# Kernel optimization log

Measured on AMD Instinct MI355X. Metric: run time of the kernel, lower is better.

The kernel has to match this reference:

```python
import jax, jax.numpy as jnp
import numpy as np

B, T, C = 4, 2048, 768   # batch, seq, n_embd
E, K = 8, 2              # n_routed_experts, moe_top_k (expert hidden dim == C per source)


def setup_inputs() -> dict:
    key = jax.random.key(0)
    ks = jax.random.split(key, 6)
    s = 0.02  # init scale to keep relu(x)^2 well-behaved
    return {
        "x": jax.random.normal(ks[0], (B, T, C), jnp.float32),
        "w_fc_sh": jax.random.normal(ks[1], (C, C), jnp.float32) * s,    # shared expert c_fc (stored [in,out])
        "w_proj_sh": jax.random.normal(ks[2], (C, C), jnp.float32) * s,  # shared expert c_proj
        "w1": jax.random.normal(ks[3], (E, C, C), jnp.float32) * s,      # routed experts c_fc, [E,in,out]
        "w2": jax.random.normal(ks[4], (E, C, C), jnp.float32) * s,      # routed experts c_proj
        "router_w": jax.random.normal(ks[5], (E, C), jnp.float32) * s,   # router weight [E, C]
        "balance_bias": jnp.zeros((E,), jnp.float32),                    # router balance_bias buffer
    }


def _mlp(x, wfc, wproj):
    # MLP: c_proj(relu(c_fc(x))**2)
    h = jnp.square(jax.nn.relu(x @ wfc))
    return h @ wproj


def reference(x, w_fc_sh, w_proj_sh, w1, w2, router_w, balance_bias):
    Bx, Tx, Cx = x.shape
    shared = _mlp(x, w_fc_sh, w_proj_sh)                    # [B,T,C]

    xf = x.reshape(-1, Cx)                                  # [N,C]
    # --- router ---
    logits = xf.astype(jnp.float32) @ router_w.T            # [N,E]
    scores = jax.nn.sigmoid(logits)
    _, idx = jax.lax.top_k(scores + balance_bias, K)        # selection uses biased scores
    tw = jnp.take_along_axis(scores, idx, axis=-1)          # gate weights from unbiased scores
    tw = tw / (tw.sum(-1, keepdims=True) + 1e-20)           # [N,K]

    # per-token per-expert combine weights (equivalent to gather/MLP/index_add loop)
    combine = (jax.nn.one_hot(idx, E, dtype=tw.dtype) * tw[..., None]).sum(1)  # [N,E]

    # dense all-expert compute, masked combine (same math as sparse dispatch)
    h = jnp.square(jax.nn.relu(jnp.einsum('nc,ech->neh', xf, w1)))  # [N,E,H]
    y = jnp.einsum('neh,ehc->nec', h, w2)                            # [N,E,C]
    routed = jnp.einsum('nec,ne->nc', y, combine)                    # [N,C]

    return shared + routed.reshape(Bx, Tx, Cx)
```

## Files before the change

### kernel.cpp

```cpp
#include <hip/hip_runtime.h>
#include <stdint.h>

#define N_TOK 8192
#define C_DIM 768
#define E_NUM 8
#define NT (C_DIM / 32)
#define TOTX 200
#define GRID1 1200
#define XXPX 25

typedef short short8 __attribute__((ext_vector_type(8)));
typedef __bf16 bf16x8 __attribute__((ext_vector_type(8)));
typedef float f32x4 __attribute__((ext_vector_type(4)));

static __device__ __forceinline__ unsigned short f2bf(float f) {
    unsigned u = __float_as_uint(f);
    unsigned r = u + 0x7FFFu + ((u >> 16) & 1u);
    return (unsigned short)(r >> 16);
}
static __device__ __forceinline__ float bf2f(unsigned short h) {
    return __uint_as_float(((unsigned)h) << 16);
}

__global__ void wtrans_kernel(const float* __restrict__ wfc, const float* __restrict__ wpj,
                              const float* __restrict__ w1, const float* __restrict__ w2,
                              unsigned short* __restrict__ Wt) {
    __shared__ float tile[32][33];
    const int m = blockIdx.z;
    const float* src = (m == 0) ? wfc : (m == 1) ? wpj
                     : (m < 10) ? (w1 + (size_t)(m - 2) * C_DIM * C_DIM)
                                : (w2 + (size_t)(m - 10) * C_DIM * C_DIM);
    const int i0 = blockIdx.y * 32;
    const int o0 = blockIdx.x * 32;
    #pragma unroll
    for (int rr = 0; rr < 32; rr += 8)
        tile[threadIdx.y + rr][threadIdx.x] = src[(size_t)(i0 + threadIdx.y + rr) * C_DIM + o0 + threadIdx.x];
    __syncthreads();
    unsigned short* dst = Wt + (size_t)m * C_DIM * C_DIM;
    #pragma unroll
    for (int rr = 0; rr < 32; rr += 8) {
        int o = o0 + threadIdx.y + rr;
        dst[(size_t)o * C_DIM + i0 + threadIdx.x] = f2bf(tile[threadIdx.x][threadIdx.y + rr]);
    }
}

__global__ void router_kernel(const float* __restrict__ x, const float* __restrict__ rw,
                              const float* __restrict__ bias,
                              float* __restrict__ topk_w, int* __restrict__ eids,
                              unsigned short* __restrict__ xb) {
    const int wave = threadIdx.x >> 6;
    const int lane = threadIdx.x & 63;
    const int n = blockIdx.x * 4 + wave;
    const float* xp = x + (size_t)n * C_DIM + lane * 12;
    float xv[12];
    #pragma unroll
    for (int j = 0; j < 12; j++) xv[j] = xp[j];
    unsigned short* xbp = xb + (size_t)n * C_DIM + lane * 12;
    #pragma unroll
    for (int j = 0; j < 12; j++) xbp[j] = f2bf(xv[j]);
    float acc[E_NUM];
    #pragma unroll
    for (int e = 0; e < E_NUM; e++) acc[e] = 0.f;
    #pragma unroll
    for (int e = 0; e < E_NUM; e++) {
        const float* wp = rw + (size_t)e * C_DIM + lane * 12;
        #pragma unroll
        for (int j = 0; j < 12; j++) acc[e] += xv[j] * wp[j];
    }
    #pragma unroll
    for (int e = 0; e < E_NUM; e++) {
        #pragma unroll
        for (int off = 32; off > 0; off >>= 1) acc[e] += __shfl_xor(acc[e], off, 64);
    }
    if (lane == 0) {
        float sc[E_NUM];
        #pragma unroll
        for (int e = 0; e < E_NUM; e++) sc[e] = 1.f / (1.f + expf(-acc[e]));
        int e0 = 0; float best = -1e30f;
        #pragma unroll
        for (int e = 0; e < E_NUM; e++) { float v = sc[e] + bias[e]; if (v > best) { best = v; e0 = e; } }
        int e1 = -1; float best1 = -1e30f;
        #pragma unroll
        for (int e = 0; e < E_NUM; e++) { if (e == e0) continue; float v = sc[e] + bias[e]; if (v > best1) { best1 = v; e1 = e; } }
        float w0 = sc[e0], w1 = sc[e1];
        float s = w0 + w1 + 1e-20f;
        w0 /= s; w1 /= s;
        topk_w[n * 2] = w0; topk_w[n * 2 + 1] = w1;
        eids[n * 2] = e0; eids[n * 2 + 1] = e1;
    }
}

__global__ __launch_bounds__(1024) void bucketize_kernel(const int* __restrict__ eids,
                                                         int* __restrict__ counts,
                                                         int* __restrict__ buckets) {
    const int e = blockIdx.x;
    const int t = threadIdx.x;
    const int wv = t >> 6, lane = t & 63;
    __shared__ int wave_tot[16];
    int running = 0;
    for (int start = 0; start < 2 * N_TOK; start += 1024) {
        const int i = start + t;
        const int f = (eids[i] == e) ? 1 : 0;
        unsigned long long mask = __ballot(f);
        int pre = __popcll(mask & ((1ull << lane) - 1ull));
        if (lane == 0) wave_tot[wv] = __popcll(mask);
        __syncthreads();
        int wbase = 0, tot = 0;
        #pragma unroll
        for (int j = 0; j < 16; j++) { int c = wave_tot[j]; tot += c; if (j < wv) wbase += c; }
        if (f) buckets[e * N_TOK + running + wbase + pre] = i;
        running += tot;
        __syncthreads();
    }
    if (t == 0) counts[e] = running;
}

__global__ void prefix_kernel(const int* __restrict__ counts, int* __restrict__ xoffs) {
    if (threadIdx.x == 0 && blockIdx.x == 0) {
        int a = 0;
        for (int z = 0; z < E_NUM; z++) { xoffs[z] = a; a += (counts[z] + 127) >> 7; }
        xoffs[E_NUM] = a;
        xoffs[E_NUM + 1] = a + 64;
    }
}

#define GLOAD_LDS(g, l) __builtin_amdgcn_global_load_lds((const __attribute__((address_space(1))) void*)(g), (__attribute__((address_space(3))) void*)(l), 16, 0, 0)
#define WAITVM(n) asm volatile("s_waitcnt vmcnt(" #n ")" ::: "memory")
#define SCHEDB() __builtin_amdgcn_sched_barrier(0)
#define BAR() __builtin_amdgcn_s_barrier()

template <int PHASE>
__global__ __launch_bounds__(256) void gemm_all_kernel(const unsigned short* __restrict__ Adir,
                                                       const unsigned short* __restrict__ Agat,
                                                       const unsigned short* __restrict__ WtAll,
                                                       void* __restrict__ dstDir,
                                                       unsigned short* __restrict__ dstGat,
                                                       const int* __restrict__ counts,
                                                       const int* __restrict__ buckets,
                                                       const int* __restrict__ xoffs) {
    const int fid = blockIdx.x;
    const int xcd = fid & 7;
    const int i6 = fid >> 3;
    const int xx = xcd * XXPX + i6 / 6;
    const int y = i6 % 6;
    int xo[10];
    #pragma unroll
    for (int i = 0; i < 10; i++) xo[i] = xoffs[i];
    if (xx >= xo[9]) return;
    int z = E_NUM, xl = xx - xo[8];
    #pragma unroll
    for (int zz = 0; zz < E_NUM; zz++)
        if (xx >= xo[zz] && xx < xo[zz + 1]) { z = zz; xl = xx - xo[zz]; }
    const bool sh = (z == E_NUM);
    const int rows = sh ? N_TOK : counts[z];
    const int r0 = xl * 128;
    const int c0 = y * 128;

    __shared__ __align__(16) unsigned short lds[4 * 8192];

    const int t = threadIdx.x;
    const int lane = t & 63;
    const int wv = t >> 6;
    const int wr = (wv >> 1) * 64;
    const int wc = (wv & 1) * 64;

    const int widx = sh ? (PHASE == 0 ? 0 : 1) : (PHASE == 0 ? 2 + z : 10 + z);
    const unsigned short* Bmat = WtAll + (size_t)widx * C_DIM * C_DIM;
    const int* bk = buckets + z * N_TOK;

    const int ar0 = t >> 2;
    const int ar1 = 64 + (t >> 2);
    const int acol = (((t & 3) ^ ((t >> 3) & 3)) * 8);
    int grow0, grow1;
    const unsigned short* Asrc;
    if (sh) {
        Asrc = Adir;
        grow0 = r0 + ar0; grow1 = r0 + ar1;
    } else {
        Asrc = Agat;
        int p0 = r0 + ar0, p1 = r0 + ar1;
        int e0v = bk[p0 < rows ? p0 : 0];
        int e1v = bk[p1 < rows ? p1 : 0];
        grow0 = (PHASE == 0) ? (e0v >> 1) : e0v;
        grow1 = (PHASE == 0) ? (e1v >> 1) : e1v;
    }
    const unsigned short* aptr0 = Asrc + (size_t)grow0 * C_DIM + acol;
    const unsigned short* aptr1 = Asrc + (size_t)grow1 * C_DIM + acol;
    const unsigned short* bptr0 = Bmat + (size_t)(c0 + ar0) * C_DIM + acol;
    const unsigned short* bptr1 = Bmat + (size_t)(c0 + ar1) * C_DIM + acol;

    f32x4 acc[4][4];
    #pragma unroll
    for (int i = 0; i < 4; i++)
        #pragma unroll
        for (int j = 0; j < 4; j++) acc[i][j] = (f32x4){0.f, 0.f, 0.f, 0.f};

    const int qr = (((lane >> 4) ^ ((lane >> 1) & 3)) * 8);

    {
        unsigned short* d0 = lds + t * 8;
        GLOAD_LDS(aptr0, d0);
        GLOAD_LDS(aptr1, d0 + 2048);
        GLOAD_LDS(bptr0, d0 + 4096);
        GLOAD_LDS(bptr1, d0 + 6144);
        unsigned short* d1 = lds + 8192 + t * 8;
        GLOAD_LDS(aptr0 + 32, d1);
        GLOAD_LDS(aptr1 + 32, d1 + 2048);
        GLOAD_LDS(bptr0 + 32, d1 + 4096);
        GLOAD_LDS(bptr1 + 32, d1 + 6144);
    }

    #pragma unroll
    for (int kt = 0; kt < NT; ++kt) {
        if (kt + 2 < NT) {
            unsigned short* d = lds + ((kt + 2) & 3) * 8192 + t * 8;
            const int ko = (kt + 2) * 32;
            GLOAD_LDS(aptr0 + ko, d);
            GLOAD_LDS(aptr1 + ko, d + 2048);
            GLOAD_LDS(bptr0 + ko, d + 4096);
            GLOAD_LDS(bptr1 + ko, d + 6144);
            WAITVM(8);
        } else if (kt + 2 == NT) {
            WAITVM(4);
        } else {
            WAITVM(0);
        }
        BAR();
        SCHEDB();
        const unsigned short* buf = lds + (kt & 3) * 8192;
        short8 af[4], bfr[4];
        #pragma unroll
        for (int i = 0; i < 4; i++)
            af[i] = *reinterpret_cast<const short8*>(buf + (size_t)(wr + i * 16 + (lane & 15)) * 32 + qr);
        #pragma unroll
        for (int j = 0; j < 4; j++)
            bfr[j] = *reinterpret_cast<const short8*>(buf + 4096 + (size_t)(wc + j * 16 + (lane & 15)) * 32 + qr);
        __builtin_amdgcn_s_setprio(1);
        #pragma unroll
        for (int i = 0; i < 4; i++)
            #pragma unroll
            for (int j = 0; j < 4; j++)
                acc[i][j] = __builtin_amdgcn_mfma_f32_16x16x32_bf16(
                    __builtin_bit_cast(bf16x8, af[i]), __builtin_bit_cast(bf16x8, bfr[j]), acc[i][j], 0, 0, 0);
        __builtin_amdgcn_s_setprio(0);
    }

    const int fr = lane & 15;
    const int fq = lane >> 4;
    if (sh) {
        if constexpr (PHASE == 0) {
            unsigned short* Hd = (unsigned short*)dstDir;
            #pragma unroll
            for (int i = 0; i < 4; i++)
                #pragma unroll
                for (int rr = 0; rr < 4; rr++) {
                    int n = r0 + wr + i * 16 + fq * 4 + rr;
                    size_t base = (size_t)n * C_DIM;
                    #pragma unroll
                    for (int j = 0; j < 4; j++) {
                        int col = c0 + wc + j * 16 + fr;
                        float v = acc[i][j][rr];
                        float rl = v > 0.f ? v : 0.f;
                        Hd[base + col] = f2bf(rl * rl);
                    }
                }
        } else {
            float* od = (float*)dstDir;
            #pragma unroll
            for (int i = 0; i < 4; i++)
                #pragma unroll
                for (int rr = 0; rr < 4; rr++) {
                    int n = r0 + wr + i * 16 + fq * 4 + rr;
                    size_t base = (size_t)n * C_DIM;
                    #pragma unroll
                    for (int j = 0; j < 4; j++) {
                        int col = c0 + wc + j * 16 + fr;
                        od[base + col] = acc[i][j][rr];
                    }
                }
        }
    } else {
        #pragma unroll
        for (int i = 0; i < 4; i++)
            #pragma unroll
            for (int rr = 0; rr < 4; rr++) {
                int pos = r0 + wr + i * 16 + fq * 4 + rr;
                if (pos < rows) {
                    int ent = bk[pos];
                    size_t base = (size_t)ent * C_DIM;
                    #pragma unroll
                    for (int j = 0; j < 4; j++) {
                        int col = c0 + wc + j * 16 + fr;
                        float v = acc[i][j][rr];
                        if (PHASE == 0) {
                            float rl = v > 0.f ? v : 0.f;
                            dstGat[base + col] = f2bf(rl * rl);
                        } else {
                            dstGat[base + col] = f2bf(v);
                        }
                    }
                }
            }
    }
}

__global__ void combine_kernel(float* __restrict__ out, const unsigned short* __restrict__ Y,
                               const float* __restrict__ tw) {
    int idx = blockIdx.x * blockDim.x + threadIdx.x;
    const int per_row = C_DIM / 4;
    if (idx >= N_TOK * per_row) return;
    int n = idx / per_row;
    int c = (idx % per_row) * 4;
    float w0 = tw[n * 2], w1 = tw[n * 2 + 1];
    const ushort4 a = *reinterpret_cast<const ushort4*>(Y + (size_t)(n * 2) * C_DIM + c);
    const ushort4 b = *reinterpret_cast<const ushort4*>(Y + (size_t)(n * 2 + 1) * C_DIM + c);
    float4* op = reinterpret_cast<float4*>(out + (size_t)n * C_DIM + c);
    float4 o = *op;
    o.x += w0 * bf2f(a.x) + w1 * bf2f(b.x);
    o.y += w0 * bf2f(a.y) + w1 * bf2f(b.y);
    o.z += w0 * bf2f(a.z) + w1 * bf2f(b.z);
    o.w += w0 * bf2f(a.w) + w1 * bf2f(b.w);
    *op = o;
}

extern "C" void kernel_launch(void* const* d_in, const int* in_sizes, int n_in,
                              void* d_out, int out_size, void* d_ws, size_t ws_size,
                              hipStream_t stream) {
    const float* x   = (const float*)d_in[0];
    const float* wfc = (const float*)d_in[1];
    const float* wpj = (const float*)d_in[2];
    const float* w1  = (const float*)d_in[3];
    const float* w2  = (const float*)d_in[4];
    const float* rw  = (const float*)d_in[5];
    const float* bias= (const float*)d_in[6];
    float* out = (float*)d_out;

    char* ws = (char*)d_ws;
    size_t off = 0;
    auto alloc = [&](size_t bytes) { void* p = ws + off; off += (bytes + 255) & ~(size_t)255; return p; };
    unsigned short* xb   = (unsigned short*)alloc((size_t)N_TOK * C_DIM * 2);
    unsigned short* Wt   = (unsigned short*)alloc((size_t)18 * C_DIM * C_DIM * 2);
    unsigned short* H    = (unsigned short*)alloc((size_t)N_TOK * 2 * C_DIM * 2);
    unsigned short* Hsh  = (unsigned short*)alloc((size_t)N_TOK * C_DIM * 2);
    unsigned short* Y    = (unsigned short*)alloc((size_t)N_TOK * 2 * C_DIM * 2);
    float* topk_w        = (float*)alloc((size_t)N_TOK * 2 * 4);
    int* counts          = (int*)alloc(256);
    int* buckets         = (int*)alloc((size_t)E_NUM * N_TOK * 4);
    int* eids            = (int*)alloc((size_t)2 * N_TOK * 4);
    int* xoffs           = (int*)alloc(64);

    wtrans_kernel<<<dim3(24, 24, 18), dim3(32, 8), 0, stream>>>(wfc, wpj, w1, w2, Wt);
    router_kernel<<<N_TOK / 4, 256, 0, stream>>>(x, rw, bias, topk_w, eids, xb);
    bucketize_kernel<<<E_NUM, 1024, 0, stream>>>(eids, counts, buckets);
    prefix_kernel<<<1, 64, 0, stream>>>(counts, xoffs);

    gemm_all_kernel<0><<<GRID1, 256, 0, stream>>>(xb, xb, Wt, Hsh, H, counts, buckets, xoffs);
    gemm_all_kernel<1><<<GRID1, 256, 0, stream>>>(Hsh, H, Wt, out, Y, counts, buckets, xoffs);

    combine_kernel<<<(N_TOK * (C_DIM / 4) + 255) / 256, 256, 0, stream>>>(out, Y, topk_w);
}
```

Measured before the change: 145.5 us.

## Use BK=64 double-buffered LDS pipeline in expert GEMM with 2-block occupancy hint

Changes the GEMM K-loop from 32-wide k-tiles with a 4-stage LDS ring (prefetch distance 2) to 64-wide k-tiles with two LDS buffers. Each buffer is loaded with an 8-way XOR swizzle, and the prefetch is issued right after the barrier. This halves the number of barriers and waitcnt points per tile and doubles the MFMA work between synchronisations. It also adds a launch_bounds minimum of 2 blocks per CU. The trade-off is shallower prefetch, since a full wait happens every iteration, which can expose more memory latency.

```diff
diff --git a/kernel.cpp b/kernel.cpp
--- a/kernel.cpp
+++ b/kernel.cpp
@@ -4,7 +4,7 @@
 #define N_TOK 8192
 #define C_DIM 768
 #define E_NUM 8
-#define NT (C_DIM / 32)
+#define NT2 (C_DIM / 64)
 #define TOTX 200
 #define GRID1 1200
 #define XXPX 25
@@ -125,19 +125,19 @@
 }
 
 #define GLOAD_LDS(g, l) __builtin_amdgcn_global_load_lds((const __attribute__((address_space(1))) void*)(g), (__attribute__((address_space(3))) void*)(l), 16, 0, 0)
-#define WAITVM(n) asm volatile("s_waitcnt vmcnt(" #n ")" ::: "memory")
+#define WAITVM0() asm volatile("s_waitcnt vmcnt(0)" ::: "memory")
 #define SCHEDB() __builtin_amdgcn_sched_barrier(0)
 #define BAR() __builtin_amdgcn_s_barrier()
 
 template <int PHASE>
-__global__ __launch_bounds__(256) void gemm_all_kernel(const unsigned short* __restrict__ Adir,
-                                                       const unsigned short* __restrict__ Agat,
-                                                       const unsigned short* __restrict__ WtAll,
-                                                       void* __restrict__ dstDir,
-                                                       unsigned short* __restrict__ dstGat,
-                                                       const int* __restrict__ counts,
-                                                       const int* __restrict__ buckets,
-                                                       const int* __restrict__ xoffs) {
+__global__ __launch_bounds__(256, 2) void gemm_all_kernel(const unsigned short* __restrict__ Adir,
+                                                          const unsigned short* __restrict__ Agat,
+                                                          const unsigned short* __restrict__ WtAll,
+                                                          void* __restrict__ dstDir,
+                                                          unsigned short* __restrict__ dstGat,
+                                                          const int* __restrict__ counts,
+                                                          const int* __restrict__ buckets,
+                                                          const int* __restrict__ xoffs) {
     const int fid = blockIdx.x;
     const int xcd = fid & 7;
     const int i6 = fid >> 3;
@@ -156,7 +156,7 @@
     const int r0 = xl * 128;
     const int c0 = y * 128;
 
-    __shared__ __align__(16) unsigned short lds[4 * 8192];
+    __shared__ __align__(16) unsigned short lds[2 * 16384];
 
     const int t = threadIdx.x;
     const int lane = t & 63;
@@ -168,26 +168,30 @@
     const unsigned short* Bmat = WtAll + (size_t)widx * C_DIM * C_DIM;
     const int* bk = buckets + z * N_TOK;
 
-    const int ar0 = t >> 2;
-    const int ar1 = 64 + (t >> 2);
-    const int acol = (((t & 3) ^ ((t >> 3) & 3)) * 8);
-    int grow0, grow1;
+    const int srow = t >> 3;
+    const int scol = (((t & 7) ^ ((t >> 3) & 7)) * 8);
+    int grow[4];
     const unsigned short* Asrc;
     if (sh) {
         Asrc = Adir;
-        grow0 = r0 + ar0; grow1 = r0 + ar1;
+        #pragma unroll
+        for (int c = 0; c < 4; c++) grow[c] = r0 + 32 * c + srow;
     } else {
         Asrc = Agat;
-        int p0 = r0 + ar0, p1 = r0 + ar1;
-        int e0v = bk[p0 < rows ? p0 : 0];
-        int e1v = bk[p1 < rows ? p1 : 0];
-        grow0 = (PHASE == 0) ? (e0v >> 1) : e0v;
-        grow1 = (PHASE == 0) ? (e1v >> 1) : e1v;
-    }
-    const unsigned short* aptr0 = Asrc + (size_t)grow0 * C_DIM + acol;
-    const unsigned short* aptr1 = Asrc + (size_t)grow1 * C_DIM + acol;
-    const unsigned short* bptr0 = Bmat + (size_t)(c0 + ar0) * C_DIM + acol;
-    const unsigned short* bptr1 = Bmat + (size_t)(c0 + ar1) * C_DIM + acol;
+        #pragma unroll
+        for (int c = 0; c < 4; c++) {
+            int p = r0 + 32 * c + srow;
+            int ev = bk[p < rows ? p : 0];
+            grow[c] = (PHASE == 0) ? (ev >> 1) : ev;
+        }
+    }
+    const unsigned short* ap[4];
+    const unsigned short* bp[4];
+    #pragma unroll
+    for (int c = 0; c < 4; c++) {
+        ap[c] = Asrc + (size_t)grow[c] * C_DIM + scol;
+        bp[c] = Bmat + (size_t)(c0 + 32 * c + srow) * C_DIM + scol;
+    }
 
     f32x4 acc[4][4];
     #pragma unroll
@@ -195,58 +199,62 @@
         #pragma unroll
         for (int j = 0; j < 4; j++) acc[i][j] = (f32x4){0.f, 0.f, 0.f, 0.f};
 
-    const int qr = (((lane >> 4) ^ ((lane >> 1) & 3)) * 8);
+    const int fr = lane & 15;
+    const int fq = lane >> 4;
+    const int ks0 = ((fq ^ (fr & 7)) * 8);
+    const int ks1 = (((4 + fq) ^ (fr & 7)) * 8);
 
     {
-        unsigned short* d0 = lds + t * 8;
-        GLOAD_LDS(aptr0, d0);
-        GLOAD_LDS(aptr1, d0 + 2048);
-        GLOAD_LDS(bptr0, d0 + 4096);
-        GLOAD_LDS(bptr1, d0 + 6144);
-        unsigned short* d1 = lds + 8192 + t * 8;
-        GLOAD_LDS(aptr0 + 32, d1);
-        GLOAD_LDS(aptr1 + 32, d1 + 2048);
-        GLOAD_LDS(bptr0 + 32, d1 + 4096);
-        GLOAD_LDS(bptr1 + 32, d1 + 6144);
-    }
-
-    #pragma unroll
-    for (int kt = 0; kt < NT; ++kt) {
-        if (kt + 2 < NT) {
-            unsigned short* d = lds + ((kt + 2) & 3) * 8192 + t * 8;
-            const int ko = (kt + 2) * 32;
-            GLOAD_LDS(aptr0 + ko, d);
-            GLOAD_LDS(aptr1 + ko, d + 2048);
-            GLOAD_LDS(bptr0 + ko, d + 4096);
-            GLOAD_LDS(bptr1 + ko, d + 6144);
-            WAITVM(8);
-        } else if (kt + 2 == NT) {
-            WAITVM(4);
-        } else {
-            WAITVM(0);
-        }
+        unsigned short* d = lds + t * 8;
+        #pragma unroll
+        for (int c = 0; c < 4; c++) {
+            GLOAD_LDS(ap[c], d + c * 2048);
+            GLOAD_LDS(bp[c], d + 8192 + c * 2048);
+        }
+    }
+
+    #pragma unroll
+    for (int kt = 0; kt < NT2; ++kt) {
+        WAITVM0();
         BAR();
         SCHEDB();
-        const unsigned short* buf = lds + (kt & 3) * 8192;
-        short8 af[4], bfr[4];
-        #pragma unroll
-        for (int i = 0; i < 4; i++)
-            af[i] = *reinterpret_cast<const short8*>(buf + (size_t)(wr + i * 16 + (lane & 15)) * 32 + qr);
-        #pragma unroll
-        for (int j = 0; j < 4; j++)
-            bfr[j] = *reinterpret_cast<const short8*>(buf + 4096 + (size_t)(wc + j * 16 + (lane & 15)) * 32 + qr);
+        if (kt + 1 < NT2) {
+            unsigned short* d = lds + ((kt + 1) & 1) * 16384 + t * 8;
+            const int ko = (kt + 1) * 64;
+            #pragma unroll
+            for (int c = 0; c < 4; c++) {
+                GLOAD_LDS(ap[c] + ko, d + c * 2048);
+                GLOAD_LDS(bp[c] + ko, d + 8192 + c * 2048);
+            }
+        }
+        SCHEDB();
+        const unsigned short* buf = lds + (kt & 1) * 16384;
+        short8 af[4][2], bfr[4][2];
+        #pragma unroll
+        for (int i = 0; i < 4; i++) {
+            const unsigned short* rp = buf + (size_t)(wr + i * 16 + fr) * 64;
+            af[i][0] = *reinterpret_cast<const short8*>(rp + ks0);
+            af[i][1] = *reinterpret_cast<const short8*>(rp + ks1);
+        }
+        #pragma unroll
+        for (int j = 0; j < 4; j++) {
+            const unsigned short* rp = buf + 8192 + (size_t)(wc + j * 16 + fr) * 64;
+            bfr[j][0] = *reinterpret_cast<const short8*>(rp + ks0);
+            bfr[j][1] = *reinterpret_cast<const short8*>(rp + ks1);
+        }
         __builtin_amdgcn_s_setprio(1);
         #pragma unroll
-        for (int i = 0; i < 4; i++)
-            #pragma unroll
-            for (int j = 0; j < 4; j++)
-                acc[i][j] = __builtin_amdgcn_mfma_f32_16x16x32_bf16(
-                    __builtin_bit_cast(bf16x8, af[i]), __builtin_bit_cast(bf16x8, bfr[j]), acc[i][j], 0, 0, 0);
+        for (int kk = 0; kk < 2; kk++)
+            #pragma unroll
+            for (int i = 0; i < 4; i++)
+                #pragma unroll
+                for (int j = 0; j < 4; j++)
+                    acc[i][j] = __builtin_amdgcn_mfma_f32_16x16x32_bf16(
+                        __builtin_bit_cast(bf16x8, af[i][kk]), __builtin_bit_cast(bf16x8, bfr[j][kk]),
+                        acc[i][j], 0, 0, 0);
         __builtin_amdgcn_s_setprio(0);
     }
 
-    const int fr = lane & 15;
-    const int fq = lane >> 4;
     if (sh) {
         if constexpr (PHASE == 0) {
             unsigned short* Hd = (unsigned short*)dstDir;
```

New measurement: 140.2 us. 3.7% less time.
